# Kernel optimization log

Measured on AMD Instinct MI355X. Metric: run time of the kernel, lower is better.

Reference implementation:

```python
import jax, jax.numpy as jnp
import numpy as np

N, E, B = 50000, 800000, 64          # nodes, edges, graphs
D_IN, HID, OUT, HEADS = 128, 64, 32, 4
NEG_SLOPE, BN_EPS = 0.2, 1e-5


def gat_conv(x, src, dst, W, a_src, a_dst, bias):
    """PyG-style GATConv (concat heads). x:[n,din], W:[din,H*C], a_*:[H,C]."""
    n = x.shape[0]
    H, C = a_src.shape
    xl = (x @ W).reshape(n, H, C)                      # [n,H,C]
    e_s = jnp.einsum('nhc,hc->nh', xl, a_src)          # alpha_src per node
    e_d = jnp.einsum('nhc,hc->nh', xl, a_dst)          # alpha_dst per node
    e = jax.nn.leaky_relu(e_s[src] + e_d[dst], NEG_SLOPE)   # [E,H]
    m = jax.ops.segment_max(e, dst, num_segments=n)
    m = jnp.where(jnp.isfinite(m), m, 0.0)             # guard isolated nodes
    p = jnp.exp(e - m[dst])
    s = jax.ops.segment_sum(p, dst, num_segments=n)
    alpha = p / (s[dst] + 1e-16)                       # edge softmax over in-edges
    out = jax.ops.segment_sum(alpha[:, :, None] * xl[src], dst, num_segments=n)
    return out.reshape(n, H * C) + bias


def batch_norm(h, gamma, beta):
    mu = h.mean(0)
    var = h.var(0)
    return (h - mu) * jax.lax.rsqrt(var + BN_EPS) * gamma + beta


def setup_inputs() -> dict:
    key = jax.random.key(0)
    ks = jax.random.split(key, 18)
    sc = 0.05
    x = jax.random.normal(ks[0], (N, D_IN), jnp.float32)
    edge_index = jax.random.randint(ks[1], (2, E), 0, N, jnp.int32)
    batch = jnp.sort(jax.random.randint(ks[2], (N,), 0, B, jnp.int32))
    C1 = HID // HEADS
    return {
        'x': x, 'edge_index': edge_index, 'batch': batch,
        'W1': jax.random.normal(ks[3], (D_IN, HID), jnp.float32) * sc,
        'a_src1': jax.random.normal(ks[4], (HEADS, C1), jnp.float32) * sc,
        'a_dst1': jax.random.normal(ks[5], (HEADS, C1), jnp.float32) * sc,
        'b1': jnp.zeros((HID,), jnp.float32),
        'g1': jnp.ones((HID,), jnp.float32),
        'be1': jnp.zeros((HID,), jnp.float32),
        'W2': jax.random.normal(ks[6], (HID, OUT), jnp.float32) * sc,
        'a_src2': jax.random.normal(ks[7], (1, OUT), jnp.float32) * sc,
        'a_dst2': jax.random.normal(ks[8], (1, OUT), jnp.float32) * sc,
        'b2': jnp.zeros((OUT,), jnp.float32),
        'g2': jnp.ones((OUT,), jnp.float32),
        'be2': jnp.zeros((OUT,), jnp.float32),
        'fcW1': jax.random.normal(ks[9], (2 * OUT, OUT), jnp.float32) * sc,
        'fcb1': jnp.zeros((OUT,), jnp.float32),
        'fcW2': jax.random.normal(ks[10], (OUT, OUT), jnp.float32) * sc,
        'fcb2': jnp.zeros((OUT,), jnp.float32),
    }


def reference(x, edge_index, batch, W1, a_src1, a_dst1, b1, g1, be1,
              W2, a_src2, a_dst2, b2, g2, be2, fcW1, fcb1, fcW2, fcb2):
    n = x.shape[0]
    loops = jnp.arange(n, dtype=edge_index.dtype)
    src = jnp.concatenate([edge_index[0], loops])   # PyG add_self_loops
    dst = jnp.concatenate([edge_index[1], loops])

    h = gat_conv(x, src, dst, W1, a_src1, a_dst1, b1)
    h = jax.nn.relu(batch_norm(h, g1, be1))          # dropout: eval no-op
    h = gat_conv(h, src, dst, W2, a_src2, a_dst2, b2)
    node_emb = batch_norm(h, g2, be2)                # [N, OUT]

    cnt = jax.ops.segment_sum(jnp.ones((n,), node_emb.dtype), batch, num_segments=B)
    gmean = jax.ops.segment_sum(node_emb, batch, num_segments=B) / jnp.maximum(cnt, 1.0)[:, None]
    gmax = jax.ops.segment_max(node_emb, batch, num_segments=B)
    gmax = jnp.where(jnp.isfinite(gmax), gmax, 0.0)
    g = jnp.concatenate([gmean, gmax], axis=1)       # [B, 2*OUT]
    g = jax.nn.relu(g @ fcW1 + fcb1)
    graph_emb = g @ fcW2 + fcb2                      # [B, OUT]
    return node_emb, graph_emb
```

## Files before the change

### kernel.cpp

```cpp
#include <hip/hip_runtime.h>
#include <math.h>

#define N_NODES 50000
#define N_EDGES 800000
#define N_GRAPHS 64
#define D_IN 128
#define HID 64
#define OUT_C 32
#define NEG 0.2f
#define BN_EPS 1e-5f
#define N_TILES 3125
#define N_BUCKETS 196
#define BIN_CHUNK 4096
#define BIN_NB 196
#define GEMM1_NB 782
#define BUCKET_CAP 5120
#define CAP_PAD 6144
#define PHANTOM N_NODES

typedef __attribute__((ext_vector_type(8))) short short8;
typedef __attribute__((ext_vector_type(4))) float f32x4;

static __device__ inline unsigned short f2bf(float f) {
    unsigned u = __float_as_uint(f);
    u += 0x7FFF + ((u >> 16) & 1);
    return (unsigned short)(u >> 16);
}
static __device__ inline float bfus(unsigned short u) {
    return __uint_as_float((unsigned)u << 16);
}


__global__ void __launch_bounds__(256) k_front(
        const int* __restrict__ src, const int* __restrict__ dst,
        int* __restrict__ gcur, unsigned* __restrict__ ebuf,
        const float* __restrict__ x, const float* __restrict__ W1,
        const float* __restrict__ a_src1, const float* __restrict__ a_dst1,
        unsigned short* __restrict__ xl1b, float* __restrict__ esd1,
        unsigned short* __restrict__ xl2b, float* __restrict__ esd2,
        const int* __restrict__ batch, int* __restrict__ gstart,
        float* __restrict__ sp1, float* __restrict__ sp2) {
    __shared__ __align__(16) char smem[23616];
    int tid = threadIdx.x;
    int blk = blockIdx.x;

    if (blk < BIN_NB) {
        int* cnt = (int*)smem;
        int* lofs = cnt + 256;
        int* dstoff = lofs + 256;
        int* ws4 = dstoff + 256;
        unsigned* stage = (unsigned*)(ws4 + 4);
        unsigned char* stage_b = (unsigned char*)(stage + BIN_CHUNK);
        cnt[tid] = 0;
        __syncthreads();
        int e0 = blk * BIN_CHUNK;
        int ne = N_EDGES - e0; if (ne > BIN_CHUNK) ne = BIN_CHUNK;
        unsigned rec[16]; int bkt[16], lp[16];
        #pragma unroll
        for (int j = 0; j < 16; ++j) {
            int r = j * 256 + tid;
            if (r < ne) {
                int e = e0 + r;
                int s = src[e], d = dst[e];
                rec[j] = ((unsigned)s << 8) | (unsigned)(d & 255);
                bkt[j] = d >> 8;
                lp[j] = atomicAdd(&cnt[bkt[j]], 1);
            } else bkt[j] = -1;
        }
        __syncthreads();
        int v = cnt[tid];
        int lane = tid & 63, wid = tid >> 6;
        int incl = v;
        #pragma unroll
        for (int off = 1; off < 64; off <<= 1) {
            int t = __shfl_up(incl, off, 64);
            if (lane >= off) incl += t;
        }
        if (lane == 63) ws4[wid] = incl;
        __syncthreads();
        if (tid == 0) {
            int a = ws4[0];
            #pragma unroll
            for (int j = 1; j < 4; ++j) { a += ws4[j]; ws4[j] = a; }
        }
        __syncthreads();
        if (wid > 0) incl += ws4[wid - 1];
        lofs[tid] = incl - v;
        __syncthreads();
        #pragma unroll
        for (int j = 0; j < 16; ++j) {
            if (bkt[j] >= 0) {
                int idx = lofs[bkt[j]] + lp[j];
                stage[idx] = rec[j];
                stage_b[idx] = (unsigned char)bkt[j];
            }
        }
        if (tid < N_BUCKETS && cnt[tid] > 0) {
            int g = atomicAdd(&gcur[tid], cnt[tid]);
            dstoff[tid] = tid * BUCKET_CAP + g - lofs[tid];
        }
        __syncthreads();
        for (int i = tid; i < ne; i += 256) {
            int b = stage_b[i];
            ebuf[dstoff[b] + i] = stage[i];
        }
        return;
    }

    if (blk < BIN_NB + GEMM1_NB) {
        typedef unsigned short WtRow[144];
        WtRow* Wt = (WtRow*)smem;
        for (int i = tid; i < 80 * 128; i += 256) {
            int n = i >> 7, k = i & 127;
            float v;
            if (n < 64) v = W1[k * 64 + n];
            else if (n < 72) {
                int hh = (n - 64) & 3;
                const float* a = ((n - 64) < 4 ? a_src1 : a_dst1) + hh * 16;
                v = 0.f;
                #pragma unroll
                for (int c = 0; c < 16; ++c) v = fmaf(W1[k * 64 + hh * 16 + c], a[c], v);
            } else v = 0.f;
            Wt[n][k] = f2bf(v);
        }
        __syncthreads();
        int lane = tid & 63, wid = tid >> 6;
        int tile = (blk - BIN_NB) * 4 + wid;
        if (tile >= N_TILES) return;
        int m = lane & 15, kg = lane >> 4;
        int base = tile * 16;
        const float* xr = x + (size_t)(base + m) * D_IN + kg * 8;
        f32x4 acc[5];
        #pragma unroll
        for (int t = 0; t < 5; ++t) acc[t] = (f32x4){0.f, 0.f, 0.f, 0.f};
        #pragma unroll
        for (int s = 0; s < 4; ++s) {
            f32x4 p = ((const f32x4*)(xr + s * 32))[0];
            f32x4 q = ((const f32x4*)(xr + s * 32))[1];
            short8 a;
            a[0] = (short)f2bf(p[0]); a[1] = (short)f2bf(p[1]);
            a[2] = (short)f2bf(p[2]); a[3] = (short)f2bf(p[3]);
            a[4] = (short)f2bf(q[0]); a[5] = (short)f2bf(q[1]);
            a[6] = (short)f2bf(q[2]); a[7] = (short)f2bf(q[3]);
            #pragma unroll
            for (int t = 0; t < 5; ++t) {
                short8 b = *(const short8*)&Wt[t * 16 + m][s * 32 + kg * 8];
                acc[t] = __builtin_amdgcn_mfma_f32_16x16x32_bf16(a, b, acc[t], 0, 0, 0);
            }
        }
        #pragma unroll
        for (int r = 0; r < 4; ++r) {
            int node = base + kg * 4 + r;
            #pragma unroll
            for (int t = 0; t < 4; ++t)
                xl1b[(size_t)node * HID + t * 16 + m] = f2bf(acc[t][r]);
            if (m < 8) esd1[node * 8 + m] = acc[4][r];
        }
        return;
    }

    if (tid <= N_GRAPHS) {
        int g = tid;
        int lo = 0, hi = N_NODES;
        while (lo < hi) {
            int mid = (lo + hi) >> 1;
            if (batch[mid] < g) lo = mid + 1; else hi = mid;
        }
        gstart[g] = lo;
    }
    if (tid >= 128 && tid < 192) xl1b[(size_t)PHANTOM * HID + (tid - 128)] = 0;
    if (tid >= 192 && tid < 200) esd1[(size_t)PHANTOM * 8 + (tid - 192)] = -1e30f;
    if (tid >= 200 && tid < 232) xl2b[(size_t)PHANTOM * OUT_C + (tid - 200)] = 0;
    if (tid >= 232 && tid < 234) esd2[(size_t)PHANTOM * 2 + (tid - 232)] = -1e30f;
    for (int i = tid; i < 64 * 128; i += 256) sp1[i] = 0.f;
    for (int i = tid; i < 64 * 64; i += 256) sp2[i] = 0.f;
}


__global__ void __launch_bounds__(256) k_csr(
        const unsigned* __restrict__ ebuf, const int* __restrict__ gcur,
        int2* __restrict__ rowinfo, int* __restrict__ col) {
    __shared__ int lcnt[256], lofs[256], lcur[256];
    __shared__ int ws[4];
    int tid = threadIdx.x, b = blockIdx.x;
    lcnt[tid] = 0;
    __syncthreads();
    int ne = gcur[b];
    const unsigned* eb = ebuf + (size_t)b * BUCKET_CAP;
    for (int i = tid; i < ne; i += 256)
        atomicAdd(&lcnt[eb[i] & 255u], 1);
    __syncthreads();
    int raw = lcnt[tid];
    int v = (raw + 3) & ~3;
    int lane = tid & 63, wid = tid >> 6;
    int incl = v;
    #pragma unroll
    for (int off = 1; off < 64; off <<= 1) {
        int t = __shfl_up(incl, off, 64);
        if (lane >= off) incl += t;
    }
    if (lane == 63) ws[wid] = incl;
    __syncthreads();
    if (tid == 0) {
        int a = ws[0];
        #pragma unroll
        for (int j = 1; j < 4; ++j) { a += ws[j]; ws[j] = a; }
    }
    __syncthreads();
    if (wid > 0) incl += ws[wid - 1];
    int js = b * CAP_PAD + (incl - v);
    int node = b * 256 + tid;
    if (node < N_NODES) rowinfo[node] = make_int2(js, js + v);
    lofs[tid] = js;
    lcur[tid] = 0;
    __syncthreads();
    for (int i = tid; i < ne; i += 256) {
        unsigned e = eb[i];
        int li = e & 255u;
        int p = atomicAdd(&lcur[li], 1);
        col[lofs[li] + p] = (int)(e >> 8);
    }
    for (int j = raw; j < v; ++j) col[js + j] = PHANTOM;
}


__global__ void __launch_bounds__(256) k_agg1(
        const unsigned short* __restrict__ xl1b, const float* __restrict__ esd1,
        const int2* __restrict__ rowinfo, const int* __restrict__ col,
        const float* __restrict__ b1, float* __restrict__ h1pre,
        float* __restrict__ sp1) {
    __shared__ float ps[64], pq[64];
    int tid = threadIdx.x;
    if (tid < 64) { ps[tid] = 0.f; pq[tid] = 0.f; }
    __syncthreads();
    int wid = tid >> 6, lane = tid & 63;
    int d = blockIdx.x * 4 + wid;
    int h = lane >> 4;
    float edh = esd1[d * 8 + 4 + h];
    float e0 = esd1[d * 8 + h] + edh;
    float w0 = __expf(fmaxf(e0, NEG * e0));
    float acc = w0 * bfus(xl1b[(size_t)d * HID + lane]);
    float wsum = w0;
    int2 ri = rowinfo[d];
    int jb = __builtin_amdgcn_readfirstlane(ri.x);
    int je = __builtin_amdgcn_readfirstlane(ri.y);
    int j = jb;
    for (; j + 8 <= je; j += 8) {
        int4 ca = *(const int4*)(col + j);
        int4 cb = *(const int4*)(col + j + 4);
        float x0 = bfus(xl1b[(size_t)ca.x * HID + lane]);
        float x1 = bfus(xl1b[(size_t)ca.y * HID + lane]);
        float x2 = bfus(xl1b[(size_t)ca.z * HID + lane]);
        float x3 = bfus(xl1b[(size_t)ca.w * HID + lane]);
        float x4 = bfus(xl1b[(size_t)cb.x * HID + lane]);
        float x5 = bfus(xl1b[(size_t)cb.y * HID + lane]);
        float x6 = bfus(xl1b[(size_t)cb.z * HID + lane]);
        float x7 = bfus(xl1b[(size_t)cb.w * HID + lane]);
        float g0 = esd1[ca.x * 8 + h] + edh;
        float g1 = esd1[ca.y * 8 + h] + edh;
        float g2 = esd1[ca.z * 8 + h] + edh;
        float g3 = esd1[ca.w * 8 + h] + edh;
        float g4 = esd1[cb.x * 8 + h] + edh;
        float g5 = esd1[cb.y * 8 + h] + edh;
        float g6 = esd1[cb.z * 8 + h] + edh;
        float g7 = esd1[cb.w * 8 + h] + edh;
        float w_0 = __expf(fmaxf(g0, NEG * g0));
        float w_1 = __expf(fmaxf(g1, NEG * g1));
        float w_2 = __expf(fmaxf(g2, NEG * g2));
        float w_3 = __expf(fmaxf(g3, NEG * g3));
        float w_4 = __expf(fmaxf(g4, NEG * g4));
        float w_5 = __expf(fmaxf(g5, NEG * g5));
        float w_6 = __expf(fmaxf(g6, NEG * g6));
        float w_7 = __expf(fmaxf(g7, NEG * g7));
        acc = fmaf(w_0, x0, acc); acc = fmaf(w_1, x1, acc);
        acc = fmaf(w_2, x2, acc); acc = fmaf(w_3, x3, acc);
        acc = fmaf(w_4, x4, acc); acc = fmaf(w_5, x5, acc);
        acc = fmaf(w_6, x6, acc); acc = fmaf(w_7, x7, acc);
        wsum += (w_0 + w_1) + (w_2 + w_3) + (w_4 + w_5) + (w_6 + w_7);
    }
    if (j < je) {
        int4 ca = *(const int4*)(col + j);
        float x0 = bfus(xl1b[(size_t)ca.x * HID + lane]);
        float x1 = bfus(xl1b[(size_t)ca.y * HID + lane]);
        float x2 = bfus(xl1b[(size_t)ca.z * HID + lane]);
        float x3 = bfus(xl1b[(size_t)ca.w * HID + lane]);
        float g0 = esd1[ca.x * 8 + h] + edh;
        float g1 = esd1[ca.y * 8 + h] + edh;
        float g2 = esd1[ca.z * 8 + h] + edh;
        float g3 = esd1[ca.w * 8 + h] + edh;
        float w_0 = __expf(fmaxf(g0, NEG * g0));
        float w_1 = __expf(fmaxf(g1, NEG * g1));
        float w_2 = __expf(fmaxf(g2, NEG * g2));
        float w_3 = __expf(fmaxf(g3, NEG * g3));
        acc = fmaf(w_0, x0, acc); acc = fmaf(w_1, x1, acc);
        acc = fmaf(w_2, x2, acc); acc = fmaf(w_3, x3, acc);
        wsum += (w_0 + w_1) + (w_2 + w_3);
    }
    float r = acc / wsum + b1[lane];
    h1pre[(size_t)d * HID + lane] = r;
    atomicAdd(&ps[lane], r);
    atomicAdd(&pq[lane], r * r);
    __syncthreads();
    int slot = (blockIdx.x & 63) * 128;
    if (tid < 64) atomicAdd(&sp1[slot + tid], ps[tid]);
    else if (tid < 128) atomicAdd(&sp1[slot + tid], pq[tid - 64]);
}


__global__ void __launch_bounds__(256) k_gemm2(
        const float* __restrict__ h1pre, const float* __restrict__ sp1,
        const float* __restrict__ g1, const float* __restrict__ be1,
        const float* __restrict__ W2, const float* __restrict__ a_src2,
        const float* __restrict__ a_dst2,
        unsigned short* __restrict__ xl2b, float* __restrict__ esd2) {
    __shared__ unsigned short Wt[48][80];
    __shared__ float A1s[64], B1s[64], red[128];
    int tid = threadIdx.x;
    for (int i = tid; i < 48 * 64; i += 256) {
        int n = i >> 6, k = i & 63;
        float v;
        if (n < 32) v = W2[k * 32 + n];
        else if (n < 34) {
            const float* a = (n == 32) ? a_src2 : a_dst2;
            v = 0.f;
            #pragma unroll
            for (int c = 0; c < 32; ++c) v = fmaf(W2[k * 32 + c], a[c], v);
        } else v = 0.f;
        Wt[n][k] = f2bf(v);
    }
    if (tid < 128) {
        float s = 0.f;
        for (int j = 0; j < 64; ++j) s += sp1[j * 128 + tid];
        red[tid] = s;
    }
    __syncthreads();
    if (tid < 64) {
        float mu = red[tid] * (1.f / N_NODES);
        float var = red[64 + tid] * (1.f / N_NODES) - mu * mu;
        float sc = g1[tid] * rsqrtf(var + BN_EPS);
        A1s[tid] = sc;
        B1s[tid] = be1[tid] - mu * sc;
    }
    __syncthreads();
    int lane = tid & 63, wid = tid >> 6;
    int tile = blockIdx.x * 4 + wid;
    if (tile >= N_TILES) return;
    int m = lane & 15, kg = lane >> 4;
    int base = tile * 16;
    const float* hr = h1pre + (size_t)(base + m) * HID + kg * 8;
    f32x4 acc[3];
    #pragma unroll
    for (int t = 0; t < 3; ++t) acc[t] = (f32x4){0.f, 0.f, 0.f, 0.f};
    #pragma unroll
    for (int s = 0; s < 2; ++s) {
        int k0 = s * 32 + kg * 8;
        f32x4 p = ((const f32x4*)(hr + s * 32))[0];
        f32x4 q = ((const f32x4*)(hr + s * 32))[1];
        f32x4 sa = *(const f32x4*)&A1s[k0];
        f32x4 sb = *(const f32x4*)&B1s[k0];
        f32x4 sa2 = *(const f32x4*)&A1s[k0 + 4];
        f32x4 sb2 = *(const f32x4*)&B1s[k0 + 4];
        short8 a;
        #pragma unroll
        for (int j = 0; j < 4; ++j) {
            float v = fmaf(p[j], sa[j], sb[j]);
            a[j] = (short)f2bf(v > 0.f ? v : 0.f);
        }
        #pragma unroll
        for (int j = 0; j < 4; ++j) {
            float v = fmaf(q[j], sa2[j], sb2[j]);
            a[4 + j] = (short)f2bf(v > 0.f ? v : 0.f);
        }
        #pragma unroll
        for (int t = 0; t < 3; ++t) {
            short8 b = *(const short8*)&Wt[t * 16 + m][s * 32 + kg * 8];
            acc[t] = __builtin_amdgcn_mfma_f32_16x16x32_bf16(a, b, acc[t], 0, 0, 0);
        }
    }
    #pragma unroll
    for (int r = 0; r < 4; ++r) {
        int node = base + kg * 4 + r;
        #pragma unroll
        for (int t = 0; t < 2; ++t)
            xl2b[(size_t)node * OUT_C + t * 16 + m] = f2bf(acc[t][r]);
        if (m < 2) esd2[node * 2 + m] = acc[2][r];
    }
}


__global__ void __launch_bounds__(256) k_agg2(
        const unsigned short* __restrict__ xl2b, const float* __restrict__ esd2,
        const int2* __restrict__ rowinfo, const int* __restrict__ col,
        const float* __restrict__ b2, float* __restrict__ h2pre,
        float* __restrict__ sp2) {
    __shared__ float ps[32], pq[32];
    int tid = threadIdx.x;
    if (tid < 32) { ps[tid] = 0.f; pq[tid] = 0.f; }
    __syncthreads();
    int wid = tid >> 6, lane = tid & 63;
    int d = blockIdx.x * 4 + wid;
    int c2 = lane & 31, half = lane >> 5;
    float edh = esd2[d * 2 + 1];
    float acc = 0.f, wsum = 0.f;
    if (half == 0) {
        float e0 = esd2[d * 2] + edh;
        float w0 = __expf(fmaxf(e0, NEG * e0));
        acc = w0 * bfus(xl2b[(size_t)d * OUT_C + c2]);
        wsum = w0;
    }
    int2 ri = rowinfo[d];
    int jb = __builtin_amdgcn_readfirstlane(ri.x);
    int je = __builtin_amdgcn_readfirstlane(ri.y);
    int j = jb;
    for (; j + 8 <= je; j += 8) {
        int4 ca = *(const int4*)(col + j);
        int4 cb = *(const int4*)(col + j + 4);
        int s0 = half ? ca.y : ca.x;
        int s1 = half ? ca.w : ca.z;
        int s2 = half ? cb.y : cb.x;
        int s3 = half ? cb.w : cb.z;
        float x0 = bfus(xl2b[(size_t)s0 * OUT_C + c2]);
        float x1 = bfus(xl2b[(size_t)s1 * OUT_C + c2]);
        float x2 = bfus(xl2b[(size_t)s2 * OUT_C + c2]);
        float x3 = bfus(xl2b[(size_t)s3 * OUT_C + c2]);
        float g0 = esd2[s0 * 2] + edh;
        float g1 = esd2[s1 * 2] + edh;
        float g2 = esd2[s2 * 2] + edh;
        float g3 = esd2[s3 * 2] + edh;
        float w_0 = __expf(fmaxf(g0, NEG * g0));
        float w_1 = __expf(fmaxf(g1, NEG * g1));
        float w_2 = __expf(fmaxf(g2, NEG * g2));
        float w_3 = __expf(fmaxf(g3, NEG * g3));
        acc = fmaf(w_0, x0, acc); acc = fmaf(w_1, x1, acc);
        acc = fmaf(w_2, x2, acc); acc = fmaf(w_3, x3, acc);
        wsum += (w_0 + w_1) + (w_2 + w_3);
    }
    if (j < je) {
        int4 ca = *(const int4*)(col + j);
        int s0 = half ? ca.y : ca.x;
        int s1 = half ? ca.w : ca.z;
        float x0 = bfus(xl2b[(size_t)s0 * OUT_C + c2]);
        float x1 = bfus(xl2b[(size_t)s1 * OUT_C + c2]);
        float g0 = esd2[s0 * 2] + edh;
        float g1 = esd2[s1 * 2] + edh;
        float w_0 = __expf(fmaxf(g0, NEG * g0));
        float w_1 = __expf(fmaxf(g1, NEG * g1));
        acc = fmaf(w_0, x0, acc); acc = fmaf(w_1, x1, acc);
        wsum += w_0 + w_1;
    }
    acc += __shfl_xor(acc, 32, 64);
    wsum += __shfl_xor(wsum, 32, 64);
    if (half == 0) {
        float r = acc / wsum + b2[c2];
        h2pre[(size_t)d * OUT_C + c2] = r;
        atomicAdd(&ps[c2], r);
        atomicAdd(&pq[c2], r * r);
    }
    __syncthreads();
    int slot = (blockIdx.x & 63) * 64;
    if (tid < 32) atomicAdd(&sp2[slot + tid], ps[tid]);
    else if (tid < 64) atomicAdd(&sp2[slot + tid], pq[tid - 32]);
}


__global__ void __launch_bounds__(256) k_bnpool(
        const float* __restrict__ h2pre, const float* __restrict__ sp2,
        const float* __restrict__ g2, const float* __restrict__ be2,
        const int* __restrict__ gstart, float* __restrict__ out,
        float* __restrict__ pfeat) {
    __shared__ float A2[OUT_C], B2[OUT_C], red[64];
    int tid = threadIdx.x;
    if (tid < 64) {
        float s = 0.f;
        for (int j = 0; j < 64; ++j) s += sp2[j * 64 + tid];
        red[tid] = s;
    }
    __syncthreads();
    if (tid < 32) {
        float mu = red[tid] * (1.f / N_NODES);
        float var = red[32 + tid] * (1.f / N_NODES) - mu * mu;
        float sc = g2[tid] * rsqrtf(var + BN_EPS);
        A2[tid] = sc;
        B2[tid] = be2[tid] - mu * sc;
    }
    __syncthreads();
    int g = blockIdx.x >> 2, part = blockIdx.x & 3;
    int s = gstart[g], e = gstart[g + 1];
    int len = e - s;
    int qq = (len + 3) >> 2;
    int ps = s + part * qq;
    int pe = ps + qq; if (pe > e) pe = e;
    int c = tid & 31, r = tid >> 5;
    float sum = 0.f, mx = -INFINITY;
    for (int n = ps + r; n < pe; n += 8) {
        float v = fmaf(h2pre[(size_t)n * OUT_C + c], A2[c], B2[c]);
        out[(size_t)n * OUT_C + c] = v;
        sum += v;
        mx = fmaxf(mx, v);
    }
    __shared__ float lsum[256], lmax[256];
    lsum[tid] = sum;
    lmax[tid] = mx;
    __syncthreads();
    if (tid < 32) {
        float ts = 0.f, tm = -INFINITY;
        for (int rr = 0; rr < 8; ++rr) {
            ts += lsum[rr * 32 + c];
            tm = fmaxf(tm, lmax[rr * 32 + c]);
        }
        pfeat[blockIdx.x * 64 + c] = ts;
        pfeat[blockIdx.x * 64 + 32 + c] = tm;
    }
}


__global__ void __launch_bounds__(256) k_mlp(
        const float* __restrict__ pfeat, const int* __restrict__ gstart,
        const float* __restrict__ fcW1, const float* __restrict__ fcb1,
        const float* __restrict__ fcW2, const float* __restrict__ fcb2,
        float* __restrict__ out) {
    __shared__ float gf[N_GRAPHS * 64];
    __shared__ float t1[N_GRAPHS * OUT_C];
    int tid = threadIdx.x;
    for (int i = tid; i < N_GRAPHS * 32; i += 256) {
        int g = i >> 5, c = i & 31;
        float sm = 0.f, mx = -INFINITY;
        #pragma unroll
        for (int p = 0; p < 4; ++p) {
            sm += pfeat[(g * 4 + p) * 64 + c];
            mx = fmaxf(mx, pfeat[(g * 4 + p) * 64 + 32 + c]);
        }
        int cnt = gstart[g + 1] - gstart[g];
        gf[g * 64 + c] = (cnt > 0) ? sm / (float)cnt : 0.f;
        gf[g * 64 + 32 + c] = (cnt > 0) ? mx : 0.f;
    }
    __syncthreads();
    for (int i = tid; i < N_GRAPHS * OUT_C; i += 256) {
        int g = i >> 5, j = i & 31;
        float a = fcb1[j];
        for (int k = 0; k < 64; ++k) a = fmaf(gf[g * 64 + k], fcW1[k * OUT_C + j], a);
        t1[i] = a > 0.f ? a : 0.f;
    }
    __syncthreads();
    for (int i = tid; i < N_GRAPHS * OUT_C; i += 256) {
        int g = i >> 5, oc = i & 31;
        float a = fcb2[oc];
        for (int k = 0; k < OUT_C; ++k) a = fmaf(t1[g * OUT_C + k], fcW2[k * OUT_C + oc], a);
        out[(size_t)N_NODES * OUT_C + g * OUT_C + oc] = a;
    }
}


extern "C" void kernel_launch(void* const* d_in, const int* in_sizes, int n_in,
                              void* d_out, int out_size, void* d_ws, size_t ws_size,
                              hipStream_t stream) {
    (void)in_sizes; (void)n_in; (void)out_size; (void)ws_size;
    const float* x      = (const float*)d_in[0];
    const int*   ei     = (const int*)d_in[1];
    const int*   batch  = (const int*)d_in[2];
    const float* W1     = (const float*)d_in[3];
    const float* a_src1 = (const float*)d_in[4];
    const float* a_dst1 = (const float*)d_in[5];
    const float* b1     = (const float*)d_in[6];
    const float* g1     = (const float*)d_in[7];
    const float* be1    = (const float*)d_in[8];
    const float* W2     = (const float*)d_in[9];
    const float* a_src2 = (const float*)d_in[10];
    const float* a_dst2 = (const float*)d_in[11];
    const float* b2     = (const float*)d_in[12];
    const float* g2     = (const float*)d_in[13];
    const float* be2    = (const float*)d_in[14];
    const float* fcW1   = (const float*)d_in[15];
    const float* fcb1   = (const float*)d_in[16];
    const float* fcW2   = (const float*)d_in[17];
    const float* fcb2   = (const float*)d_in[18];
    const int* srcv = ei;
    const int* dstv = ei + N_EDGES;
    float* out = (float*)d_out;

    char* w = (char*)d_ws;
    size_t o = 0;
    #define ALLOC(nbytes) (w + o); o = (o + (size_t)(nbytes) + 15) & ~(size_t)15
    int*   gcur      = (int*)ALLOC(N_BUCKETS * 4);
    size_t zero_bytes = o;
    float* sp1       = (float*)ALLOC(64 * 128 * 4);
    float* sp2       = (float*)ALLOC(64 * 64 * 4);
    int2*  rowinfo   = (int2*)ALLOC((size_t)N_NODES * 8);
    int*   gst       = (int*)ALLOC(66 * 4);
    int*   col       = (int*)ALLOC(((size_t)N_BUCKETS * CAP_PAD + 256) * 4);
    unsigned* ebuf   = (unsigned*)ALLOC((size_t)N_BUCKETS * BUCKET_CAP * 4);
    unsigned short* xl1b = (unsigned short*)ALLOC((size_t)(N_NODES + 1) * HID * 2);
    float* esd1      = (float*)ALLOC((size_t)(N_NODES + 1) * 8 * 4);
    float* h1pre     = (float*)ALLOC((size_t)N_NODES * HID * 4);
    unsigned short* xl2b = (unsigned short*)ALLOC((size_t)(N_NODES + 1) * OUT_C * 2);
    float* esd2      = (float*)ALLOC((size_t)(N_NODES + 1) * 2 * 4);
    float* pfeat     = (float*)ALLOC(256 * 64 * 4);
    #undef ALLOC
    float* h2pre = h1pre;

    hipMemsetAsync(d_ws, 0, zero_bytes, stream);
    k_front <<<BIN_NB + GEMM1_NB + 1, 256, 0, stream>>>(
        srcv, dstv, gcur, ebuf, x, W1, a_src1, a_dst1,
        xl1b, esd1, xl2b, esd2, batch, gst, sp1, sp2);
    k_csr   <<<N_BUCKETS, 256, 0, stream>>>(ebuf, gcur, rowinfo, col);
    k_agg1  <<<N_NODES / 4, 256, 0, stream>>>(
        xl1b, esd1, rowinfo, col, b1, h1pre, sp1);
    k_gemm2 <<<(N_TILES + 3) / 4, 256, 0, stream>>>(
        h1pre, sp1, g1, be1, W2, a_src2, a_dst2, xl2b, esd2);
    k_agg2  <<<N_NODES / 4, 256, 0, stream>>>(
        xl2b, esd2, rowinfo, col, b2, h2pre, sp2);
    k_bnpool<<<256, 256, 0, stream>>>(h2pre, sp2, g2, be2, gst, out, pfeat);
    k_mlp   <<<1, 256, 0, stream>>>(pfeat, gst, fcW1, fcb1, fcW2, fcb2, out);
}
```

Baseline: 263.9 us.

## Make GAT aggregation kernels persistent with grid-stride nodes and prefetched column indices

Both aggregation kernels now launch a fixed 1024 blocks, and each wave walks nodes in a grid-stride loop instead of handling one node per wave. Each wave keeps BatchNorm sum and sum-of-squares in registers and issues a single shared atomic at the end, instead of one per node. The next group of eight column indices is loaded one iteration ahead so that index loads overlap the gathers. In exchange, fewer waves are resident to hide gather latency, per-wave work varies with node degree, and the prefetch can read past a row's end into padded memory.

```diff
diff --git a/kernel.cpp b/kernel.cpp
--- a/kernel.cpp
+++ b/kernel.cpp
@@ -17,6 +17,8 @@
 #define BUCKET_CAP 5120
 #define CAP_PAD 6144
 #define PHANTOM N_NODES
+#define AGG_NB 1024
+#define N_WAVES (AGG_NB * 4)
 
 typedef __attribute__((ext_vector_type(8))) short short8;
 typedef __attribute__((ext_vector_type(4))) float f32x4;
@@ -234,72 +236,80 @@
     if (tid < 64) { ps[tid] = 0.f; pq[tid] = 0.f; }
     __syncthreads();
     int wid = tid >> 6, lane = tid & 63;
-    int d = blockIdx.x * 4 + wid;
+    int wave = blockIdx.x * 4 + wid;
     int h = lane >> 4;
-    float edh = esd1[d * 8 + 4 + h];
-    float e0 = esd1[d * 8 + h] + edh;
-    float w0 = __expf(fmaxf(e0, NEG * e0));
-    float acc = w0 * bfus(xl1b[(size_t)d * HID + lane]);
-    float wsum = w0;
-    int2 ri = rowinfo[d];
-    int jb = __builtin_amdgcn_readfirstlane(ri.x);
-    int je = __builtin_amdgcn_readfirstlane(ri.y);
-    int j = jb;
-    for (; j + 8 <= je; j += 8) {
-        int4 ca = *(const int4*)(col + j);
-        int4 cb = *(const int4*)(col + j + 4);
-        float x0 = bfus(xl1b[(size_t)ca.x * HID + lane]);
-        float x1 = bfus(xl1b[(size_t)ca.y * HID + lane]);
-        float x2 = bfus(xl1b[(size_t)ca.z * HID + lane]);
-        float x3 = bfus(xl1b[(size_t)ca.w * HID + lane]);
-        float x4 = bfus(xl1b[(size_t)cb.x * HID + lane]);
-        float x5 = bfus(xl1b[(size_t)cb.y * HID + lane]);
-        float x6 = bfus(xl1b[(size_t)cb.z * HID + lane]);
-        float x7 = bfus(xl1b[(size_t)cb.w * HID + lane]);
-        float g0 = esd1[ca.x * 8 + h] + edh;
-        float g1 = esd1[ca.y * 8 + h] + edh;
-        float g2 = esd1[ca.z * 8 + h] + edh;
-        float g3 = esd1[ca.w * 8 + h] + edh;
-        float g4 = esd1[cb.x * 8 + h] + edh;
-        float g5 = esd1[cb.y * 8 + h] + edh;
-        float g6 = esd1[cb.z * 8 + h] + edh;
-        float g7 = esd1[cb.w * 8 + h] + edh;
-        float w_0 = __expf(fmaxf(g0, NEG * g0));
-        float w_1 = __expf(fmaxf(g1, NEG * g1));
-        float w_2 = __expf(fmaxf(g2, NEG * g2));
-        float w_3 = __expf(fmaxf(g3, NEG * g3));
-        float w_4 = __expf(fmaxf(g4, NEG * g4));
-        float w_5 = __expf(fmaxf(g5, NEG * g5));
-        float w_6 = __expf(fmaxf(g6, NEG * g6));
-        float w_7 = __expf(fmaxf(g7, NEG * g7));
-        acc = fmaf(w_0, x0, acc); acc = fmaf(w_1, x1, acc);
-        acc = fmaf(w_2, x2, acc); acc = fmaf(w_3, x3, acc);
-        acc = fmaf(w_4, x4, acc); acc = fmaf(w_5, x5, acc);
-        acc = fmaf(w_6, x6, acc); acc = fmaf(w_7, x7, acc);
-        wsum += (w_0 + w_1) + (w_2 + w_3) + (w_4 + w_5) + (w_6 + w_7);
-    }
-    if (j < je) {
-        int4 ca = *(const int4*)(col + j);
-        float x0 = bfus(xl1b[(size_t)ca.x * HID + lane]);
-        float x1 = bfus(xl1b[(size_t)ca.y * HID + lane]);
-        float x2 = bfus(xl1b[(size_t)ca.z * HID + lane]);
-        float x3 = bfus(xl1b[(size_t)ca.w * HID + lane]);
-        float g0 = esd1[ca.x * 8 + h] + edh;
-        float g1 = esd1[ca.y * 8 + h] + edh;
-        float g2 = esd1[ca.z * 8 + h] + edh;
-        float g3 = esd1[ca.w * 8 + h] + edh;
-        float w_0 = __expf(fmaxf(g0, NEG * g0));
-        float w_1 = __expf(fmaxf(g1, NEG * g1));
-        float w_2 = __expf(fmaxf(g2, NEG * g2));
-        float w_3 = __expf(fmaxf(g3, NEG * g3));
-        acc = fmaf(w_0, x0, acc); acc = fmaf(w_1, x1, acc);
-        acc = fmaf(w_2, x2, acc); acc = fmaf(w_3, x3, acc);
-        wsum += (w_0 + w_1) + (w_2 + w_3);
-    }
-    float r = acc / wsum + b1[lane];
-    h1pre[(size_t)d * HID + lane] = r;
-    atomicAdd(&ps[lane], r);
-    atomicAdd(&pq[lane], r * r);
+    float bl = b1[lane];
+    float s = 0.f, q = 0.f;
+    for (int d = wave; d < N_NODES; d += N_WAVES) {
+        float edh = esd1[d * 8 + 4 + h];
+        float e0 = esd1[d * 8 + h] + edh;
+        float w0 = __expf(fmaxf(e0, NEG * e0));
+        float acc = w0 * bfus(xl1b[(size_t)d * HID + lane]);
+        float wsum = w0;
+        int2 ri = rowinfo[d];
+        int jb = __builtin_amdgcn_readfirstlane(ri.x);
+        int je = __builtin_amdgcn_readfirstlane(ri.y);
+        int4 ca = *(const int4*)(col + jb);
+        int4 cb = *(const int4*)(col + jb + 4);
+        int j = jb;
+        for (; j + 8 <= je; j += 8) {
+            int4 na = *(const int4*)(col + j + 8);
+            int4 nb = *(const int4*)(col + j + 12);
+            float x0 = bfus(xl1b[(size_t)ca.x * HID + lane]);
+            float x1 = bfus(xl1b[(size_t)ca.y * HID + lane]);
+            float x2 = bfus(xl1b[(size_t)ca.z * HID + lane]);
+            float x3 = bfus(xl1b[(size_t)ca.w * HID + lane]);
+            float x4 = bfus(xl1b[(size_t)cb.x * HID + lane]);
+            float x5 = bfus(xl1b[(size_t)cb.y * HID + lane]);
+            float x6 = bfus(xl1b[(size_t)cb.z * HID + lane]);
+            float x7 = bfus(xl1b[(size_t)cb.w * HID + lane]);
+            float g0 = esd1[ca.x * 8 + h] + edh;
+            float g1 = esd1[ca.y * 8 + h] + edh;
+            float g2 = esd1[ca.z * 8 + h] + edh;
+            float g3 = esd1[ca.w * 8 + h] + edh;
+            float g4 = esd1[cb.x * 8 + h] + edh;
+            float g5 = esd1[cb.y * 8 + h] + edh;
+            float g6 = esd1[cb.z * 8 + h] + edh;
+            float g7 = esd1[cb.w * 8 + h] + edh;
+            float w_0 = __expf(fmaxf(g0, NEG * g0));
+            float w_1 = __expf(fmaxf(g1, NEG * g1));
+            float w_2 = __expf(fmaxf(g2, NEG * g2));
+            float w_3 = __expf(fmaxf(g3, NEG * g3));
+            float w_4 = __expf(fmaxf(g4, NEG * g4));
+            float w_5 = __expf(fmaxf(g5, NEG * g5));
+            float w_6 = __expf(fmaxf(g6, NEG * g6));
+            float w_7 = __expf(fmaxf(g7, NEG * g7));
+            acc = fmaf(w_0, x0, acc); acc = fmaf(w_1, x1, acc);
+            acc = fmaf(w_2, x2, acc); acc = fmaf(w_3, x3, acc);
+            acc = fmaf(w_4, x4, acc); acc = fmaf(w_5, x5, acc);
+            acc = fmaf(w_6, x6, acc); acc = fmaf(w_7, x7, acc);
+            wsum += (w_0 + w_1) + (w_2 + w_3) + (w_4 + w_5) + (w_6 + w_7);
+            ca = na; cb = nb;
+        }
+        if (j < je) {
+            float x0 = bfus(xl1b[(size_t)ca.x * HID + lane]);
+            float x1 = bfus(xl1b[(size_t)ca.y * HID + lane]);
+            float x2 = bfus(xl1b[(size_t)ca.z * HID + lane]);
+            float x3 = bfus(xl1b[(size_t)ca.w * HID + lane]);
+            float g0 = esd1[ca.x * 8 + h] + edh;
+            float g1 = esd1[ca.y * 8 + h] + edh;
+            float g2 = esd1[ca.z * 8 + h] + edh;
+            float g3 = esd1[ca.w * 8 + h] + edh;
+            float w_0 = __expf(fmaxf(g0, NEG * g0));
+            float w_1 = __expf(fmaxf(g1, NEG * g1));
+            float w_2 = __expf(fmaxf(g2, NEG * g2));
+            float w_3 = __expf(fmaxf(g3, NEG * g3));
+            acc = fmaf(w_0, x0, acc); acc = fmaf(w_1, x1, acc);
+            acc = fmaf(w_2, x2, acc); acc = fmaf(w_3, x3, acc);
+            wsum += (w_0 + w_1) + (w_2 + w_3);
+        }
+        float r = acc / wsum + bl;
+        h1pre[(size_t)d * HID + lane] = r;
+        s += r;
+        q = fmaf(r, r, q);
+    }
+    atomicAdd(&ps[lane], s);
+    atomicAdd(&pq[lane], q);
     __syncthreads();
     int slot = (blockIdx.x & 63) * 128;
     if (tid < 64) atomicAdd(&sp1[slot + tid], ps[tid]);
@@ -398,63 +408,73 @@
     if (tid < 32) { ps[tid] = 0.f; pq[tid] = 0.f; }
     __syncthreads();
     int wid = tid >> 6, lane = tid & 63;
-    int d = blockIdx.x * 4 + wid;
+    int wave = blockIdx.x * 4 + wid;
     int c2 = lane & 31, half = lane >> 5;
-    float edh = esd2[d * 2 + 1];
-    float acc = 0.f, wsum = 0.f;
+    float bl = b2[c2];
+    float s = 0.f, q = 0.f;
+    for (int d = wave; d < N_NODES; d += N_WAVES) {
+        float edh = esd2[d * 2 + 1];
+        float acc = 0.f, wsum = 0.f;
+        if (half == 0) {
+            float e0 = esd2[d * 2] + edh;
+            float w0 = __expf(fmaxf(e0, NEG * e0));
+            acc = w0 * bfus(xl2b[(size_t)d * OUT_C + c2]);
+            wsum = w0;
+        }
+        int2 ri = rowinfo[d];
+        int jb = __builtin_amdgcn_readfirstlane(ri.x);
+        int je = __builtin_amdgcn_readfirstlane(ri.y);
+        int4 ca = *(const int4*)(col + jb);
+        int4 cb = *(const int4*)(col + jb + 4);
+        int j = jb;
+        for (; j + 8 <= je; j += 8) {
+            int4 na = *(const int4*)(col + j + 8);
+            int4 nb = *(const int4*)(col + j + 12);
+            int s0 = half ? ca.y : ca.x;
+            int s1 = half ? ca.w : ca.z;
+            int s2 = half ? cb.y : cb.x;
+            int s3 = half ? cb.w : cb.z;
+            float x0 = bfus(xl2b[(size_t)s0 * OUT_C + c2]);
+            float x1 = bfus(xl2b[(size_t)s1 * OUT_C + c2]);
+            float x2 = bfus(xl2b[(size_t)s2 * OUT_C + c2]);
+            float x3 = bfus(xl2b[(size_t)s3 * OUT_C + c2]);
+            float g0 = esd2[s0 * 2] + edh;
+            float g1 = esd2[s1 * 2] + edh;
+            float g2 = esd2[s2 * 2] + edh;
+            float g3 = esd2[s3 * 2] + edh;
+            float w_0 = __expf(fmaxf(g0, NEG * g0));
+            float w_1 = __expf(fmaxf(g1, NEG * g1));
+            float w_2 = __expf(fmaxf(g2, NEG * g2));
+            float w_3 = __expf(fmaxf(g3, NEG * g3));
+            acc = fmaf(w_0, x0, acc); acc = fmaf(w_1, x1, acc);
+            acc = fmaf(w_2, x2, acc); acc = fmaf(w_3, x3, acc);
+            wsum += (w_0 + w_1) + (w_2 + w_3);
+            ca = na; cb = nb;
+        }
+        if (j < je) {
+            int s0 = half ? ca.y : ca.x;
+            int s1 = half ? ca.w : ca.z;
+            float x0 = bfus(xl2b[(size_t)s0 * OUT_C + c2]);
+            float x1 = bfus(xl2b[(size_t)s1 * OUT_C + c2]);
+            float g0 = esd2[s0 * 2] + edh;
+            float g1 = esd2[s1 * 2] + edh;
+            float w_0 = __expf(fmaxf(g0, NEG * g0));
+            float w_1 = __expf(fmaxf(g1, NEG * g1));
+            acc = fmaf(w_0, x0, acc); acc = fmaf(w_1, x1, acc);
+            wsum += w_0 + w_1;
+        }
+        acc += __shfl_xor(acc, 32, 64);
+        wsum += __shfl_xor(wsum, 32, 64);
+        if (half == 0) {
+            float r = acc / wsum + bl;
+            h2pre[(size_t)d * OUT_C + c2] = r;
+            s += r;
+            q = fmaf(r, r, q);
+        }
+    }
     if (half == 0) {
-        float e0 = esd2[d * 2] + edh;
-        float w0 = __expf(fmaxf(e0, NEG * e0));
-        acc = w0 * bfus(xl2b[(size_t)d * OUT_C + c2]);
-        wsum = w0;
-    }
-    int2 ri = rowinfo[d];
-    int jb = __builtin_amdgcn_readfirstlane(ri.x);
-    int je = __builtin_amdgcn_readfirstlane(ri.y);
-    int j = jb;
-    for (; j + 8 <= je; j += 8) {
-        int4 ca = *(const int4*)(col + j);
-        int4 cb = *(const int4*)(col + j + 4);
-        int s0 = half ? ca.y : ca.x;
-        int s1 = half ? ca.w : ca.z;
-        int s2 = half ? cb.y : cb.x;
-        int s3 = half ? cb.w : cb.z;
-        float x0 = bfus(xl2b[(size_t)s0 * OUT_C + c2]);
-        float x1 = bfus(xl2b[(size_t)s1 * OUT_C + c2]);
-        float x2 = bfus(xl2b[(size_t)s2 * OUT_C + c2]);
-        float x3 = bfus(xl2b[(size_t)s3 * OUT_C + c2]);
-        float g0 = esd2[s0 * 2] + edh;
-        float g1 = esd2[s1 * 2] + edh;
-        float g2 = esd2[s2 * 2] + edh;
-        float g3 = esd2[s3 * 2] + edh;
-        float w_0 = __expf(fmaxf(g0, NEG * g0));
-        float w_1 = __expf(fmaxf(g1, NEG * g1));
-        float w_2 = __expf(fmaxf(g2, NEG * g2));
-        float w_3 = __expf(fmaxf(g3, NEG * g3));
-        acc = fmaf(w_0, x0, acc); acc = fmaf(w_1, x1, acc);
-        acc = fmaf(w_2, x2, acc); acc = fmaf(w_3, x3, acc);
-        wsum += (w_0 + w_1) + (w_2 + w_3);
-    }
-    if (j < je) {
-        int4 ca = *(const int4*)(col + j);
-        int s0 = half ? ca.y : ca.x;
-        int s1 = half ? ca.w : ca.z;
-        float x0 = bfus(xl2b[(size_t)s0 * OUT_C + c2]);
-        float x1 = bfus(xl2b[(size_t)s1 * OUT_C + c2]);
-        float g0 = esd2[s0 * 2] + edh;
-        float g1 = esd2[s1 * 2] + edh;
-        float w_0 = __expf(fmaxf(g0, NEG * g0));
-        float w_1 = __expf(fmaxf(g1, NEG * g1));
-        acc = fmaf(w_0, x0, acc); acc = fmaf(w_1, x1, acc);
-        wsum += w_0 + w_1;
-    }
-    acc += __shfl_xor(acc, 32, 64);
-    wsum += __shfl_xor(wsum, 32, 64);
-    if (half == 0) {
-        float r = acc / wsum + b2[c2];
-        h2pre[(size_t)d * OUT_C + c2] = r;
-        atomicAdd(&ps[c2], r);
-        atomicAdd(&pq[c2], r * r);
+        atomicAdd(&ps[c2], s);
+        atomicAdd(&pq[c2], q);
     }
     __syncthreads();
     int slot = (blockIdx.x & 63) * 64;
@@ -603,11 +623,11 @@
         srcv, dstv, gcur, ebuf, x, W1, a_src1, a_dst1,
         xl1b, esd1, xl2b, esd2, batch, gst, sp1, sp2);
     k_csr   <<<N_BUCKETS, 256, 0, stream>>>(ebuf, gcur, rowinfo, col);
-    k_agg1  <<<N_NODES / 4, 256, 0, stream>>>(
+    k_agg1  <<<AGG_NB, 256, 0, stream>>>(
         xl1b, esd1, rowinfo, col, b1, h1pre, sp1);
     k_gemm2 <<<(N_TILES + 3) / 4, 256, 0, stream>>>(
         h1pre, sp1, g1, be1, W2, a_src2, a_dst2, xl2b, esd2);
-    k_agg2  <<<N_NODES / 4, 256, 0, stream>>>(
+    k_agg2  <<<AGG_NB, 256, 0, stream>>>(
         xl2b, esd2, rowinfo, col, b2, h2pre, sp2);
     k_bnpool<<<256, 256, 0, stream>>>(h2pre, sp2, g2, be2, gst, out, pfeat);
     k_mlp   <<<1, 256, 0, stream>>>(pfeat, gst, fcW1, fcb1, fcW2, fcb2, out);
```

Result: faster. 243.6 us (-7.7%).
